# Performance work log

Measured on AMD Instinct MI355X. Metric: run time of the kernel, lower is better.

Reference implementation:

```python
import jax, jax.numpy as jnp
import numpy as np

NEG_INF = -9e15
ALPHA = 0.2  # leaky relu negative slope
N, M, F_IN, F_OUT = 20000, 64, 64, 64


def setup_inputs() -> dict:
    key = jax.random.key(0)
    k1, k2, k3, k4, k5 = jax.random.split(key, 5)
    item_embs = jax.random.normal(k1, (N, F_IN), dtype=jnp.float32)
    entity_embs = jax.random.normal(k2, (N, M, F_IN), dtype=jnp.float32)
    adj = jax.random.randint(k3, (N, M), 0, 2, dtype=jnp.int32)
    # xavier_uniform with gain=1.414
    def xavier(k, shape, gain=1.414):
        fan_in, fan_out = shape[0], shape[1]
        limit = gain * np.sqrt(6.0 / (fan_in + fan_out))
        return jax.random.uniform(k, shape, jnp.float32, -limit, limit)
    W = xavier(k4, (F_IN, F_OUT))
    a = xavier(k5, (2 * F_OUT, 1))
    return {"item_embs": item_embs, "entity_embs": entity_embs, "adj": adj, "W": W, "a": a}


def reference(item_embs, entity_embs, adj, W, a):
    # Dropouts are identity (inference mode).
    Wh = item_embs @ W                                   # [N, H]
    We = jnp.einsum('nmf,fh->nmh', entity_embs, W)       # [N, M, H]
    # cat(Wh, We) @ a  ==  Wh @ a[:H]  +  We @ a[H:]
    H = W.shape[1]
    a1, a2 = a[:H, 0], a[H:, 0]
    e = (Wh @ a1)[:, None] + We @ a2                     # [N, M]
    e = jax.nn.leaky_relu(e, negative_slope=ALPHA)
    e = jnp.where(adj > 0, e, NEG_INF)
    attention = jax.nn.softmax(e, axis=1)                # [N, M]
    # weighted aggregation of ORIGINAL entity embeddings + residual
    entity_weighted = jnp.einsum('nm,nmf->nf', attention, entity_embs)
    h_prime = entity_weighted + item_embs                # [N, F_IN]
    return h_prime  # concat=False -> no elu
```

## Files before the change

kernel.cpp:

```cpp
#include <hip/hip_runtime.h>

#define NEG_INF -9000000000000000.0f
#define ALPHA 0.2f

__global__ void precompute_wa(const float* __restrict__ W, const float* __restrict__ a,
                              float* __restrict__ wa) {
    __shared__ float a_sh[128];
    int t = threadIdx.x;
    a_sh[t] = a[t];
    __syncthreads();
    if (t < 64) {
        float s1 = 0.f, s2 = 0.f;
        const float* row = W + t * 64;
#pragma unroll
        for (int h = 0; h < 64; ++h) {
            float w = row[h];
            s1 += w * a_sh[h];
            s2 += w * a_sh[64 + h];
        }
        wa[t] = s1;
        wa[64 + t] = s2;
    }
}

__global__ __launch_bounds__(256) void gat_kernel(
    const float* __restrict__ item, const float* __restrict__ ent_g,
    const int* __restrict__ adj, const float* __restrict__ wa,
    float* __restrict__ out)
{
    __shared__ float ent[64 * 64];
    __shared__ float item_sh[64];
    __shared__ float e_sh[64];
    __shared__ float red_sh[256];
    __shared__ float s1_sh;

    const int n = blockIdx.x;
    const int t = threadIdx.x;

    const float4* src4 = (const float4*)(ent_g + (size_t)n * 4096);
    float4 v[4];
#pragma unroll
    for (int i = 0; i < 4; ++i) v[i] = src4[i * 256 + t];

    const int q = t & 15;
    const float4 w2 = ((const float4*)(wa + 64))[q];
    int adjv = 0;
    float p1 = 0.f;
    if (t < 64) {
        adjv = adj[(size_t)n * 64 + t];
        p1 = item[(size_t)n * 64 + t] * wa[t];
    } else if (t < 128) {
        item_sh[t - 64] = item[(size_t)n * 64 + (t - 64)];
    }

#pragma unroll
    for (int i = 0; i < 4; ++i) {
        ((float4*)ent)[i * 256 + t] = v[i];
        float p = v[i].x * w2.x + v[i].y * w2.y + v[i].z * w2.z + v[i].w * w2.w;
        p += __shfl_xor(p, 1);
        p += __shfl_xor(p, 2);
        p += __shfl_xor(p, 4);
        p += __shfl_xor(p, 8);
        if (q == 0) e_sh[i * 16 + (t >> 4)] = p;
    }

    if (t < 64) {
#pragma unroll
        for (int k = 1; k < 64; k <<= 1) p1 += __shfl_xor(p1, k);
        if (t == 0) s1_sh = p1;
    }
    __syncthreads();

    if (t < 64) {
        float e = s1_sh + e_sh[t];
        e = e > 0.f ? e : ALPHA * e;
        if (adjv <= 0) e = NEG_INF;
        float mx = e;
#pragma unroll
        for (int k = 1; k < 64; k <<= 1) mx = fmaxf(mx, __shfl_xor(mx, k));
        float ex = __expf(e - mx);
        float sm = ex;
#pragma unroll
        for (int k = 1; k < 64; k <<= 1) sm += __shfl_xor(sm, k);
        e_sh[t] = ex / sm;
    }
    __syncthreads();

    const int f = t & 63;
    const int g = t >> 6;
    float acc = 0.f;
#pragma unroll
    for (int mm = 0; mm < 16; ++mm) {
        const int row = g * 16 + mm;
        acc += e_sh[row] * ent[row * 64 + f];
    }
    red_sh[t] = acc;
    __syncthreads();
    if (t < 64) {
        out[(size_t)n * 64 + t] =
            red_sh[t] + red_sh[64 + t] + red_sh[128 + t] + red_sh[192 + t] + item_sh[t];
    }
}

extern "C" void kernel_launch(void* const* d_in, const int* in_sizes, int n_in,
                              void* d_out, int out_size, void* d_ws, size_t ws_size,
                              hipStream_t stream) {
    const float* item = (const float*)d_in[0];
    const float* ent  = (const float*)d_in[1];
    const int*   adj  = (const int*)d_in[2];
    const float* W    = (const float*)d_in[3];
    const float* a    = (const float*)d_in[4];
    float* out = (float*)d_out;
    float* wa  = (float*)d_ws;

    const int N = in_sizes[0] / 64;

    precompute_wa<<<1, 128, 0, stream>>>(W, a, wa);
    gat_kernel<<<N, 256, 0, stream>>>(item, ent, adj, wa, out);
}
```

Baseline: 431.8 us.

## Keep entity tile in registers and aggregate with wave shuffles instead of LDS

The 16KB shared-memory copy of each node's entity tile is removed. The weighted aggregation now uses the float4 values already held in registers, broadcasting attention weights with __shfl and reducing across row groups with xor-shuffles. Every wavefront computes the softmax redundantly, which removes one barrier and the single-wave serial phase. The intent is to cut LDS traffic and LDS footprint so more blocks fit per CU. In exchange the score and softmax work is done four times per block.

Measured after the change: 441.1 us. +2.2%, slower.

```diff
diff --git a/kernel.cpp b/kernel.cpp
--- a/kernel.cpp
+++ b/kernel.cpp
@@ -28,34 +28,27 @@
     const int* __restrict__ adj, const float* __restrict__ wa,
     float* __restrict__ out)
 {
-    __shared__ float ent[64 * 64];
-    __shared__ float item_sh[64];
     __shared__ float e_sh[64];
     __shared__ float red_sh[256];
-    __shared__ float s1_sh;
 
     const int n = blockIdx.x;
     const int t = threadIdx.x;
+    const int l = t & 63;
+    const int w = t >> 6;
+    const int q = t & 15;
 
     const float4* src4 = (const float4*)(ent_g + (size_t)n * 4096);
     float4 v[4];
 #pragma unroll
     for (int i = 0; i < 4; ++i) v[i] = src4[i * 256 + t];
 
-    const int q = t & 15;
-    const float4 w2 = ((const float4*)(wa + 64))[q];
-    int adjv = 0;
-    float p1 = 0.f;
-    if (t < 64) {
-        adjv = adj[(size_t)n * 64 + t];
-        p1 = item[(size_t)n * 64 + t] * wa[t];
-    } else if (t < 128) {
-        item_sh[t - 64] = item[(size_t)n * 64 + (t - 64)];
-    }
+    const float4 w2   = ((const float4*)(wa + 64))[q];
+    const int   adjv  = adj[(size_t)n * 64 + l];
+    const float itemv = item[(size_t)n * 64 + l];
+    const float wa1l  = wa[l];
 
 #pragma unroll
     for (int i = 0; i < 4; ++i) {
-        ((float4*)ent)[i * 256 + t] = v[i];
         float p = v[i].x * w2.x + v[i].y * w2.y + v[i].z * w2.z + v[i].w * w2.w;
         p += __shfl_xor(p, 1);
         p += __shfl_xor(p, 2);
@@ -64,41 +57,45 @@
         if (q == 0) e_sh[i * 16 + (t >> 4)] = p;
     }
 
-    if (t < 64) {
+    float s1 = itemv * wa1l;
 #pragma unroll
-        for (int k = 1; k < 64; k <<= 1) p1 += __shfl_xor(p1, k);
-        if (t == 0) s1_sh = p1;
+    for (int k = 1; k < 64; k <<= 1) s1 += __shfl_xor(s1, k);
+
+    __syncthreads();
+
+    float e = s1 + e_sh[l];
+    e = e > 0.f ? e : ALPHA * e;
+    if (adjv <= 0) e = NEG_INF;
+    float mx = e;
+#pragma unroll
+    for (int k = 1; k < 64; k <<= 1) mx = fmaxf(mx, __shfl_xor(mx, k));
+    float ex = __expf(e - mx);
+    float sm = ex;
+#pragma unroll
+    for (int k = 1; k < 64; k <<= 1) sm += __shfl_xor(sm, k);
+    const float attw = ex / sm;
+
+    float4 acc = {0.f, 0.f, 0.f, 0.f};
+#pragma unroll
+    for (int i = 0; i < 4; ++i) {
+        const int row = i * 16 + (t >> 4);
+        const float ai = __shfl(attw, row);
+        acc.x += ai * v[i].x;
+        acc.y += ai * v[i].y;
+        acc.z += ai * v[i].z;
+        acc.w += ai * v[i].w;
     }
+
+    acc.x += __shfl_xor(acc.x, 16); acc.y += __shfl_xor(acc.y, 16);
+    acc.z += __shfl_xor(acc.z, 16); acc.w += __shfl_xor(acc.w, 16);
+    acc.x += __shfl_xor(acc.x, 32); acc.y += __shfl_xor(acc.y, 32);
+    acc.z += __shfl_xor(acc.z, 32); acc.w += __shfl_xor(acc.w, 32);
+    if (l < 16) ((float4*)red_sh)[w * 16 + l] = acc;
     __syncthreads();
 
     if (t < 64) {
-        float e = s1_sh + e_sh[t];
-        e = e > 0.f ? e : ALPHA * e;
-        if (adjv <= 0) e = NEG_INF;
-        float mx = e;
-#pragma unroll
-        for (int k = 1; k < 64; k <<= 1) mx = fmaxf(mx, __shfl_xor(mx, k));
-        float ex = __expf(e - mx);
-        float sm = ex;
-#pragma unroll
-        for (int k = 1; k < 64; k <<= 1) sm += __shfl_xor(sm, k);
-        e_sh[t] = ex / sm;
-    }
-    __syncthreads();
-
-    const int f = t & 63;
-    const int g = t >> 6;
-    float acc = 0.f;
-#pragma unroll
-    for (int mm = 0; mm < 16; ++mm) {
-        const int row = g * 16 + mm;
-        acc += e_sh[row] * ent[row * 64 + f];
-    }
-    red_sh[t] = acc;
-    __syncthreads();
-    if (t < 64) {
         out[(size_t)n * 64 + t] =
-            red_sh[t] + red_sh[64 + t] + red_sh[128 + t] + red_sh[192 + t] + item_sh[t];
+            red_sh[t] + red_sh[64 + t] + red_sh[128 + t] + red_sh[192 + t] + itemv;
     }
 }
 
```
